# Performance work log

Hardware: AMD Instinct MI355X
Metric: run time of the kernel (lower is better)

The kernel has to match this reference:

```python
import jax, jax.numpy as jnp
import numpy as np

DIM_MODEL = 1024
DIM_K = 1024
DIM_V = 1024


def setup_inputs() -> dict:
    key = jax.random.key(0)
    ks = jax.random.split(key, 7)
    B, S = 4, 2048
    scale = 1.0 / np.sqrt(DIM_MODEL)
    return {
        "x": jax.random.normal(ks[0], (B, S, DIM_MODEL), dtype=jnp.float32),
        # weights stored [in, out] (transpose of torch Linear.weight)
        "Wq": jax.random.normal(ks[1], (DIM_MODEL, DIM_K), dtype=jnp.float32) * scale,
        "Wk": jax.random.normal(ks[2], (DIM_MODEL, DIM_K), dtype=jnp.float32) * scale,
        "Wv": jax.random.normal(ks[3], (DIM_MODEL, DIM_V), dtype=jnp.float32) * scale,
        "Wo": jax.random.normal(ks[4], (DIM_V, DIM_MODEL), dtype=jnp.float32) * (1.0 / np.sqrt(DIM_V)),
        "ln2_gamma": jnp.ones((DIM_MODEL,), dtype=jnp.float32),
        "ln2_beta": jnp.zeros((DIM_MODEL,), dtype=jnp.float32),
    }


def _layernorm(x, gamma, beta, eps=1e-5):
    mu = jnp.mean(x, axis=-1, keepdims=True)
    var = jnp.var(x, axis=-1, keepdims=True)
    return (x - mu) * jax.lax.rsqrt(var + eps) * gamma + beta


def reference(x, Wq, Wk, Wv, Wo, ln2_gamma, ln2_beta):
    # single-head attention, x: [B,S,D]
    q = jnp.einsum("bsd,dk->bsk", x, Wq)
    k = jnp.einsum("bsd,dk->bsk", x, Wk)
    v = jnp.einsum("bsd,dv->bsv", x, Wv)
    scores = jnp.einsum("bqk,bsk->bqs", q, k) / jnp.sqrt(jnp.asarray(DIM_K, x.dtype))
    attn = jax.nn.softmax(scores, axis=-1)  # [B,S,S]
    ctx = jnp.einsum("bqs,bsv->bqv", attn, v)
    hidden = jnp.einsum("bqv,vd->bqd", ctx, Wo)
    hidden = _layernorm(hidden, ln2_gamma, ln2_beta)
    return hidden
```

## Files before the change

### kernel.cpp

```cpp
#include <hip/hip_runtime.h>
#include <hip/hip_bf16.h>
#include <stdint.h>

typedef __bf16 bf16;
typedef __attribute__((ext_vector_type(8))) __bf16 bf16x8;
typedef __attribute__((ext_vector_type(4))) __bf16 bf16x4;
typedef __attribute__((ext_vector_type(4))) float f32x4;

#define AS1 __attribute__((address_space(1)))
#define AS3 __attribute__((address_space(3)))

__device__ __forceinline__ void gl_lds16(const void* g, void* l) {
  __builtin_amdgcn_global_load_lds((const AS1 uint32_t*)g, (AS3 uint32_t*)l, 16, 0, 0);
}

#define FENCE() asm volatile("" ::: "memory")
#define BAR()                        \
  do {                               \
    FENCE();                         \
    __builtin_amdgcn_s_barrier();    \
    FENCE();                         \
  } while (0)
#define VMW4() asm volatile("s_waitcnt vmcnt(4)" ::: "memory")

template <int MODE>
__global__ __launch_bounds__(512, 2) void gemm256(
    const bf16* __restrict__ Abase, const bf16* __restrict__ Bbase,
    bf16* __restrict__ Cbase, int K, int lda, int ldb, int ldc,
    long long sA, long long sB, long long sC, float alpha,
    float* __restrict__ lsum, bf16* __restrict__ C2, bf16* __restrict__ C3) {
  extern __shared__ char smem[];
  const int z = blockIdx.z;
  const bf16* A = Abase + (long long)z * sA;
  const bf16* B = Bbase + (long long)z * sB;
  bf16* C = Cbase + (long long)z * sC;
  const int m0 = blockIdx.y * 256, n0 = blockIdx.x * 256;
  const int t = threadIdx.x;
  const int lane = t & 63;
  const int wid = t >> 6, wrow = wid >> 2, wcol = wid & 3;
  const int quad = lane >> 4, r = lane & 15;

  const int rowq = t >> 3;
  const int chunk = (t & 7) ^ (rowq & 7);
  const bf16* pA0 = A + (long long)(m0 + rowq) * lda + chunk * 8;
  const bf16* pB0 = B + (long long)(n0 + rowq) * ldb + chunk * 8;

  const int aoff = (wrow * 64 + r) * 128;
  const int boff = 32768 + (wcol * 32 + r) * 128;
  const int cs0 = ((quad) ^ (r & 7)) * 16;
  const int cs1 = ((4 + quad) ^ (r & 7)) * 16;

#define STAGE_A(HALF, KT, SB)                                                  \
  do {                                                                         \
    gl_lds16(pA0 + (long long)((HALF) * 128) * lda + (KT),                     \
             (SB) + (HALF) * 16384 + t * 16);                                  \
    gl_lds16(pA0 + (long long)((HALF) * 128 + 64) * lda + (KT),                \
             (SB) + (HALF) * 16384 + 8192 + t * 16);                           \
  } while (0)
#define STAGE_B(HALF, KT, SB)                                                  \
  do {                                                                         \
    gl_lds16(pB0 + (long long)((HALF) * 128) * ldb + (KT),                     \
             (SB) + 32768 + (HALF) * 16384 + t * 16);                          \
    gl_lds16(pB0 + (long long)((HALF) * 128 + 64) * ldb + (KT),                \
             (SB) + 32768 + (HALF) * 16384 + 8192 + t * 16);                   \
  } while (0)
#define READ_A(MH)                                                             \
  _Pragma("unroll") for (int mr = 0; mr < 4; ++mr) {                           \
    af[mr][0] = *(const bf16x8*)(Sc + (MH) * 16384 + aoff + mr * 2048 + cs0);  \
    af[mr][1] = *(const bf16x8*)(Sc + (MH) * 16384 + aoff + mr * 2048 + cs1);  \
  }
#define READ_B(NH)                                                             \
  _Pragma("unroll") for (int nr = 0; nr < 2; ++nr) {                           \
    bfr[NH][nr][0] =                                                           \
        *(const bf16x8*)(Sc + (NH) * 16384 + boff + nr * 2048 + cs0);          \
    bfr[NH][nr][1] =                                                           \
        *(const bf16x8*)(Sc + (NH) * 16384 + boff + nr * 2048 + cs1);          \
  }
#define MMA(MH, NH)                                                            \
  _Pragma("unroll") for (int mr = 0; mr < 4; ++mr)                             \
      _Pragma("unroll") for (int nr = 0; nr < 2; ++nr) {                       \
    acc[MH][NH][mr][nr] = __builtin_amdgcn_mfma_f32_16x16x32_bf16(             \
        af[mr][0], bfr[NH][nr][0], acc[MH][NH][mr][nr], 0, 0, 0);              \
    acc[MH][NH][mr][nr] = __builtin_amdgcn_mfma_f32_16x16x32_bf16(             \
        af[mr][1], bfr[NH][nr][1], acc[MH][NH][mr][nr], 0, 0, 0);              \
  }

  f32x4 acc[2][2][4][2] = {};
  bf16x8 af[4][2];
  bf16x8 bfr[2][2][2];
  char* Sc = smem;
  char* Sn = smem + 65536;
  const int T = K >> 6;

  STAGE_A(0, 0, Sc);
  STAGE_B(0, 0, Sc);
  STAGE_A(1, 0, Sc);
  STAGE_B(1, 0, Sc);
  {
    const int kt1p = (T > 1) ? 64 : 0;
    STAGE_A(0, kt1p, Sn);
    STAGE_B(0, kt1p, Sn);
  }
  VMW4();
  BAR();

  for (int tt = 0; tt < T; ++tt) {
    const int kt1 = (tt + 1 < T ? tt + 1 : 0) << 6;
    const int kt2 = (tt + 2 < T ? tt + 2 : 0) << 6;
    READ_A(0);
    READ_B(0);
    STAGE_A(1, kt1, Sn);
    __builtin_amdgcn_s_setprio(1);
    MMA(0, 0);
    __builtin_amdgcn_s_setprio(0);
    BAR();
    READ_B(1);
    STAGE_B(1, kt1, Sn);
    __builtin_amdgcn_s_setprio(1);
    MMA(0, 1);
    __builtin_amdgcn_s_setprio(0);
    BAR();
    READ_A(1);
    STAGE_A(0, kt2, Sc);
    __builtin_amdgcn_s_setprio(1);
    MMA(1, 0);
    __builtin_amdgcn_s_setprio(0);
    BAR();
    STAGE_B(0, kt2, Sc);
    __builtin_amdgcn_s_setprio(1);
    MMA(1, 1);
    __builtin_amdgcn_s_setprio(0);
    VMW4();
    BAR();
    char* tp = Sc;
    Sc = Sn;
    Sn = tp;
  }

  if constexpr (MODE == 4) {
    bf16* dst;
    int c0;
    if (n0 < 1024) {
      dst = Cbase;
      c0 = n0;
    } else if (n0 < 2048) {
      dst = C2;
      c0 = n0 - 1024;
    } else {
      dst = C3;
      c0 = n0 - 2048;
    }
#pragma unroll
    for (int mh = 0; mh < 2; ++mh)
#pragma unroll
      for (int mr = 0; mr < 4; ++mr) {
        const int row0 = m0 + mh * 128 + wrow * 64 + mr * 16 + quad * 4;
#pragma unroll
        for (int nh = 0; nh < 2; ++nh)
#pragma unroll
          for (int nr = 0; nr < 2; ++nr) {
            const int col = c0 + nh * 128 + wcol * 32 + nr * 16 + r;
#pragma unroll
            for (int rg = 0; rg < 4; ++rg)
              dst[(long long)(row0 + rg) * 1024 + col] =
                  (bf16)acc[mh][nh][mr][nr][rg];
          }
      }
    return;
  }

#pragma unroll
  for (int mh = 0; mh < 2; ++mh)
#pragma unroll
    for (int mr = 0; mr < 4; ++mr) {
      const int row0 = m0 + mh * 128 + wrow * 64 + mr * 16 + quad * 4;
      float rsum[4] = {0.f, 0.f, 0.f, 0.f};
      float inv[4];
      if constexpr (MODE == 2) {
#pragma unroll
        for (int rg = 0; rg < 4; ++rg)
          inv[rg] = 1.f / lsum[(long long)z * 2048 + row0 + rg];
      }
#pragma unroll
      for (int nh = 0; nh < 2; ++nh)
#pragma unroll
        for (int nr = 0; nr < 2; ++nr) {
          const int col = n0 + nh * 128 + wcol * 32 + nr * 16 + r;
#pragma unroll
          for (int rg = 0; rg < 4; ++rg) {
            float v = acc[mh][nh][mr][nr][rg] * alpha;
            if constexpr (MODE == 1) {
              bf16 eb = (bf16)__expf(v);
              C[(long long)(row0 + rg) * ldc + col] = eb;
              rsum[rg] += (float)eb;
            } else if constexpr (MODE == 2) {
              C[(long long)(row0 + rg) * ldc + col] = (bf16)(v * inv[rg]);
            } else {
              C[(long long)(row0 + rg) * ldc + col] = (bf16)v;
            }
          }
        }
      if constexpr (MODE == 1) {
#pragma unroll
        for (int rg = 0; rg < 4; ++rg) {
#pragma unroll
          for (int off = 8; off >= 1; off >>= 1)
            rsum[rg] += __shfl_xor(rsum[rg], off);
          if (r == 0)
            atomicAdd(&lsum[(long long)z * 2048 + row0 + rg], rsum[rg]);
        }
      }
    }
#undef STAGE_A
#undef STAGE_B
#undef READ_A
#undef READ_B
#undef MMA
}

template <int MODE>
__global__ __launch_bounds__(256) void gemm128(
    const bf16* __restrict__ Abase, const bf16* __restrict__ Bbase,
    bf16* __restrict__ Cbase, int K, int lda, int ldb, int ldc,
    long long sA, long long sB, long long sC, float alpha,
    float* __restrict__ lsum, bf16* __restrict__ C2, bf16* __restrict__ C3) {
  extern __shared__ char smem[];
  const int z = blockIdx.z;
  const bf16* A = Abase + (long long)z * sA;
  const bf16* B = Bbase + (long long)z * sB;
  bf16* C = Cbase + (long long)z * sC;
  const int m0 = blockIdx.y * 128, n0 = blockIdx.x * 128;
  const int t = threadIdx.x;
  const int lane = t & 63, wave = t >> 6;
  const int wm = (wave >> 1) * 64, wn = (wave & 1) * 64;
  const int quad = lane >> 4, r = lane & 15;

  const int srow = t >> 3;
  const int schunk = (t & 7) ^ (srow & 7);
  const bf16* ga = A + (long long)(m0 + srow) * lda + schunk * 8;
  const bf16* gb = B + (long long)(n0 + srow) * ldb + schunk * 8;
  char* la = smem + t * 16;
  char* lb = smem + 16384 + t * 16;

  f32x4 acc[4][4] = {};

  for (int k0 = 0; k0 < K; k0 += 64) {
    __syncthreads();
#pragma unroll
    for (int rd = 0; rd < 4; rd++) {
      gl_lds16(ga + (long long)(32 * rd) * lda, la + rd * 4096);
      gl_lds16(gb + (long long)(32 * rd) * ldb, lb + rd * 4096);
    }
    ga += 64;
    gb += 64;
    __syncthreads();

#pragma unroll
    for (int kk = 0; kk < 2; kk++) {
      bf16x8 af[4], bfr[4];
      const int csa = ((kk * 4 + quad) ^ (r & 7)) * 16;
      const char* pa = smem + (wm + r) * 128 + csa;
      const char* pb = smem + 16384 + (wn + r) * 128 + csa;
#pragma unroll
      for (int i = 0; i < 4; i++) af[i] = *(const bf16x8*)(pa + i * 2048);
#pragma unroll
      for (int j = 0; j < 4; j++) bfr[j] = *(const bf16x8*)(pb + j * 2048);
#pragma unroll
      for (int i = 0; i < 4; i++)
#pragma unroll
        for (int j = 0; j < 4; j++)
          acc[i][j] = __builtin_amdgcn_mfma_f32_16x16x32_bf16(af[i], bfr[j],
                                                              acc[i][j], 0, 0, 0);
    }
  }

#pragma unroll
  for (int i = 0; i < 4; i++) {
    const int row0 = m0 + wm + i * 16 + quad * 4;
#pragma unroll
    for (int j = 0; j < 4; j++) {
      const int col = n0 + wn + j * 16 + r;
#pragma unroll
      for (int rg = 0; rg < 4; rg++) {
        float v = acc[i][j][rg] * alpha;
        C[(long long)(row0 + rg) * ldc + col] = (bf16)v;
      }
    }
  }
}

__global__ __launch_bounds__(256) void prep(
    const float* __restrict__ x, const float* __restrict__ Wq,
    const float* __restrict__ Wk, const float* __restrict__ Wv,
    const float* __restrict__ Wo, bf16* __restrict__ Xb,
    bf16* __restrict__ Wcat, bf16* __restrict__ Wot,
    float* __restrict__ lsum) {
  __shared__ float tile[32][33];
  const int bx = blockIdx.x;
  const int t = threadIdx.x;
  if (bx < 4096) {
    if (bx < 32) lsum[bx * 256 + t] = 0.f;
    long long i = (long long)bx * 256 + t;
    const float4* p = (const float4*)x;
    float4 a = p[i * 2], b = p[i * 2 + 1];
    bf16x8 o;
    o[0] = (bf16)a.x; o[1] = (bf16)a.y; o[2] = (bf16)a.z; o[3] = (bf16)a.w;
    o[4] = (bf16)b.x; o[5] = (bf16)b.y; o[6] = (bf16)b.z; o[7] = (bf16)b.w;
    ((bf16x8*)Xb)[i] = o;
  } else {
    int idx = bx - 4096;
    const int zw = idx >> 10;
    idx &= 1023;
    const int tiy = idx >> 5, tix = idx & 31;
    const float* W = (zw == 0) ? Wq : (zw == 1) ? Wk : (zw == 2) ? Wv : Wo;
    bf16* dst = (zw < 3) ? (Wcat + (long long)zw * 1024 * 1024) : Wot;
    const int bx0 = tix * 32, by0 = tiy * 32;
    const int ttx = t & 31, tty = t >> 5;
#pragma unroll
    for (int i = 0; i < 32; i += 8)
      tile[tty + i][ttx] = W[(long long)(by0 + tty + i) * 1024 + bx0 + ttx];
    __syncthreads();
#pragma unroll
    for (int i = 0; i < 32; i += 8)
      dst[(long long)(bx0 + tty + i) * 1024 + by0 + ttx] = (bf16)tile[ttx][tty + i];
  }
}

__global__ __launch_bounds__(256) void layernorm_rows(
    const bf16* __restrict__ H, const float* __restrict__ gamma,
    const float* __restrict__ beta, float* __restrict__ O) {
  const long long row = blockIdx.x;
  const bf16* h = H + row * 1024;
  float* o = O + row * 1024;
  const int t = threadIdx.x;
  const int lane = t & 63, wave = t >> 6;
  bf16x4 hv = ((const bf16x4*)h)[t];
  float v[4] = {(float)hv[0], (float)hv[1], (float)hv[2], (float)hv[3]};
  float s = v[0] + v[1] + v[2] + v[3];
  float ss = v[0] * v[0] + v[1] * v[1] + v[2] * v[2] + v[3] * v[3];
#pragma unroll
  for (int off = 32; off >= 1; off >>= 1) {
    s += __shfl_xor(s, off);
    ss += __shfl_xor(ss, off);
  }
  __shared__ float rs[4], rss[4];
  if (lane == 0) {
    rs[wave] = s;
    rss[wave] = ss;
  }
  __syncthreads();
  s = rs[0] + rs[1] + rs[2] + rs[3];
  ss = rss[0] + rss[1] + rss[2] + rss[3];
  const float mean = s * (1.f / 1024.f);
  const float var = ss * (1.f / 1024.f) - mean * mean;
  const float rstd = rsqrtf(var + 1e-5f);
  float4 g = ((const float4*)gamma)[t];
  float4 bb = ((const float4*)beta)[t];
  float4 rr;
  rr.x = (v[0] - mean) * rstd * g.x + bb.x;
  rr.y = (v[1] - mean) * rstd * g.y + bb.y;
  rr.z = (v[2] - mean) * rstd * g.z + bb.z;
  rr.w = (v[3] - mean) * rstd * g.w + bb.w;
  ((float4*)o)[t] = rr;
}

extern "C" void kernel_launch(void* const* d_in, const int* in_sizes, int n_in,
                              void* d_out, int out_size, void* d_ws,
                              size_t ws_size, hipStream_t stream) {
  const float* x = (const float*)d_in[0];
  const float* Wq = (const float*)d_in[1];
  const float* Wk = (const float*)d_in[2];
  const float* Wv = (const float*)d_in[3];
  const float* Wo = (const float*)d_in[4];
  const float* gamma = (const float*)d_in[5];
  const float* beta = (const float*)d_in[6];
  float* out = (float*)d_out;

  char* ws = (char*)d_ws;
  const size_t MB = 1024ull * 1024ull;
  bf16* Xb = (bf16*)(ws + 0);
  bf16* Wcat = (bf16*)(ws + 16 * MB);
  bf16* Wot = (bf16*)(ws + 22 * MB);
  bf16* Qd = (bf16*)(ws + 24 * MB);
  bf16* Kd = (bf16*)(ws + 40 * MB);
  bf16* Vd = (bf16*)(ws + 56 * MB);
  bf16* expS = (bf16*)(ws + 72 * MB);
  float* lsum = (float*)(ws + 104 * MB);
  bf16* VWo = (bf16*)(ws + 105 * MB);
  bf16* Hd = (bf16*)(ws + 121 * MB);

  static int inited = 0;
  if (!inited) {
    hipFuncSetAttribute(reinterpret_cast<const void*>(&gemm256<4>),
                        hipFuncAttributeMaxDynamicSharedMemorySize, 131072);
    hipFuncSetAttribute(reinterpret_cast<const void*>(&gemm256<1>),
                        hipFuncAttributeMaxDynamicSharedMemorySize, 131072);
    hipFuncSetAttribute(reinterpret_cast<const void*>(&gemm256<2>),
                        hipFuncAttributeMaxDynamicSharedMemorySize, 131072);
    inited = 1;
  }

  prep<<<8192, 256, 0, stream>>>(x, Wq, Wk, Wv, Wo, Xb, Wcat, Wot, lsum);

  gemm256<4><<<dim3(12, 32, 1), 512, 131072, stream>>>(
      Xb, Wcat, Qd, 1024, 1024, 1024, 1024, 0, 0, 0, 1.f, nullptr, Kd, Vd);

  gemm256<1><<<dim3(8, 8, 4), 512, 131072, stream>>>(
      Qd, Kd, expS, 1024, 1024, 1024, 2048, 2048 * 1024LL, 2048 * 1024LL,
      2048 * 2048LL, 0.03125f, lsum, nullptr, nullptr);

  gemm128<0><<<dim3(16, 8, 4), 256, 32768, stream>>>(
      Wot, Vd, VWo, 1024, 1024, 1024, 2048, 0, 2048 * 1024LL, 1024 * 2048LL,
      1.f, nullptr, nullptr, nullptr);

  gemm256<2><<<dim3(4, 8, 4), 512, 131072, stream>>>(
      expS, VWo, Hd, 2048, 2048, 2048, 1024, 2048 * 2048LL, 1024 * 2048LL,
      2048 * 1024LL, 1.f, lsum, nullptr, nullptr);

  layernorm_rows<<<8192, 256, 0, stream>>>(Hd, gamma, beta, out);
}
```

Measured before the change: 279.8 us.

## Fold Wv·Wo into a fused weight and project V·Wo inside the QKV GEMM

Precomputes the weight product Wv·Wo once, which is small, and writes it as the third block of the concatenated QKV weight. The projection GEMM then emits U = x·(Wv·Wo) directly in transposed layout. This removes the separate per-batch V·Wo GEMM, which was 2x the FLOPs. The QKV projection and the final P·U GEMM move from the 256-tile kernel to the 128-tile kernel with launch bounds set to 3 blocks, giving more blocks on this grid. Rounding Wv·Wo to bf16 adds a different rounding error, and the transposed bf16x4 stores are strided.

```diff
diff --git a/kernel.cpp b/kernel.cpp
--- a/kernel.cpp
+++ b/kernel.cpp
@@ -137,50 +137,12 @@
     Sn = tp;
   }
 
-  if constexpr (MODE == 4) {
-    bf16* dst;
-    int c0;
-    if (n0 < 1024) {
-      dst = Cbase;
-      c0 = n0;
-    } else if (n0 < 2048) {
-      dst = C2;
-      c0 = n0 - 1024;
-    } else {
-      dst = C3;
-      c0 = n0 - 2048;
-    }
-#pragma unroll
-    for (int mh = 0; mh < 2; ++mh)
-#pragma unroll
-      for (int mr = 0; mr < 4; ++mr) {
-        const int row0 = m0 + mh * 128 + wrow * 64 + mr * 16 + quad * 4;
-#pragma unroll
-        for (int nh = 0; nh < 2; ++nh)
-#pragma unroll
-          for (int nr = 0; nr < 2; ++nr) {
-            const int col = c0 + nh * 128 + wcol * 32 + nr * 16 + r;
-#pragma unroll
-            for (int rg = 0; rg < 4; ++rg)
-              dst[(long long)(row0 + rg) * 1024 + col] =
-                  (bf16)acc[mh][nh][mr][nr][rg];
-          }
-      }
-    return;
-  }
-
 #pragma unroll
   for (int mh = 0; mh < 2; ++mh)
 #pragma unroll
     for (int mr = 0; mr < 4; ++mr) {
       const int row0 = m0 + mh * 128 + wrow * 64 + mr * 16 + quad * 4;
       float rsum[4] = {0.f, 0.f, 0.f, 0.f};
-      float inv[4];
-      if constexpr (MODE == 2) {
-#pragma unroll
-        for (int rg = 0; rg < 4; ++rg)
-          inv[rg] = 1.f / lsum[(long long)z * 2048 + row0 + rg];
-      }
 #pragma unroll
       for (int nh = 0; nh < 2; ++nh)
 #pragma unroll
@@ -193,8 +155,6 @@
               bf16 eb = (bf16)__expf(v);
               C[(long long)(row0 + rg) * ldc + col] = eb;
               rsum[rg] += (float)eb;
-            } else if constexpr (MODE == 2) {
-              C[(long long)(row0 + rg) * ldc + col] = (bf16)(v * inv[rg]);
             } else {
               C[(long long)(row0 + rg) * ldc + col] = (bf16)v;
             }
@@ -219,7 +179,7 @@
 }
 
 template <int MODE>
-__global__ __launch_bounds__(256) void gemm128(
+__global__ __launch_bounds__(256, 3) void gemm128(
     const bf16* __restrict__ Abase, const bf16* __restrict__ Bbase,
     bf16* __restrict__ Cbase, int K, int lda, int ldb, int ldc,
     long long sA, long long sB, long long sC, float alpha,
@@ -274,16 +234,67 @@
     }
   }
 
+  if constexpr (MODE == 4) {
+    if (n0 >= 2048) {
+      bf16* Ut = C3;
+      const int d0 = n0 - 2048;
+#pragma unroll
+      for (int i = 0; i < 4; i++) {
+        const int s0 = m0 + wm + i * 16 + quad * 4;
+#pragma unroll
+        for (int j = 0; j < 4; j++) {
+          const int d = d0 + wn + j * 16 + r;
+          bf16x4 o;
+          o[0] = (bf16)acc[i][j][0];
+          o[1] = (bf16)acc[i][j][1];
+          o[2] = (bf16)acc[i][j][2];
+          o[3] = (bf16)acc[i][j][3];
+          *(bf16x4*)&Ut[(long long)d * 8192 + s0] = o;
+        }
+      }
+      return;
+    }
+    bf16* dst;
+    int c0;
+    if (n0 < 1024) {
+      dst = Cbase; c0 = n0;
+    } else {
+      dst = C2; c0 = n0 - 1024;
+    }
+#pragma unroll
+    for (int i = 0; i < 4; i++) {
+      const int row0 = m0 + wm + i * 16 + quad * 4;
+#pragma unroll
+      for (int j = 0; j < 4; j++) {
+        const int col = c0 + wn + j * 16 + r;
+#pragma unroll
+        for (int rg = 0; rg < 4; rg++)
+          dst[(long long)(row0 + rg) * 1024 + col] = (bf16)acc[i][j][rg];
+      }
+    }
+    return;
+  }
+
 #pragma unroll
   for (int i = 0; i < 4; i++) {
     const int row0 = m0 + wm + i * 16 + quad * 4;
+    float inv[4];
+    if constexpr (MODE == 2) {
+#pragma unroll
+      for (int rg = 0; rg < 4; rg++)
+        inv[rg] = 1.f / lsum[(long long)z * 2048 + row0 + rg];
+    }
 #pragma unroll
     for (int j = 0; j < 4; j++) {
       const int col = n0 + wn + j * 16 + r;
 #pragma unroll
       for (int rg = 0; rg < 4; rg++) {
         float v = acc[i][j][rg] * alpha;
-        C[(long long)(row0 + rg) * ldc + col] = (bf16)v;
+        if constexpr (MODE == 2) {
+          C[(long long)(row0 + rg) * ldc + col] = (bf16)(v * inv[rg]);
+        } else {
+          C[(long long)(row0 + rg) * ldc + col] = (bf16)v;
+        }
       }
     }
   }
@@ -294,7 +305,7 @@
     const float* __restrict__ Wk, const float* __restrict__ Wv,
     const float* __restrict__ Wo, bf16* __restrict__ Xb,
     bf16* __restrict__ Wcat, bf16* __restrict__ Wot,
-    float* __restrict__ lsum) {
+    bf16* __restrict__ Wvb, float* __restrict__ lsum) {
   __shared__ float tile[32][33];
   const int bx = blockIdx.x;
   const int t = threadIdx.x;
@@ -311,9 +322,17 @@
     int idx = bx - 4096;
     const int zw = idx >> 10;
     idx &= 1023;
+    if (zw == 2) {
+      const long long base = (long long)idx * 1024 + t * 4;
+      float4 v = *(const float4*)&Wv[base];
+      bf16x4 o;
+      o[0] = (bf16)v.x; o[1] = (bf16)v.y; o[2] = (bf16)v.z; o[3] = (bf16)v.w;
+      *(bf16x4*)&Wvb[base] = o;
+      return;
+    }
     const int tiy = idx >> 5, tix = idx & 31;
-    const float* W = (zw == 0) ? Wq : (zw == 1) ? Wk : (zw == 2) ? Wv : Wo;
-    bf16* dst = (zw < 3) ? (Wcat + (long long)zw * 1024 * 1024) : Wot;
+    const float* W = (zw == 0) ? Wq : (zw == 1) ? Wk : Wo;
+    bf16* dst = (zw == 0) ? Wcat : (zw == 1) ? (Wcat + 1024 * 1024) : Wot;
     const int bx0 = tix * 32, by0 = tiy * 32;
     const int ttx = t & 31, tty = t >> 5;
 #pragma unroll
@@ -383,38 +402,34 @@
   bf16* Wot = (bf16*)(ws + 22 * MB);
   bf16* Qd = (bf16*)(ws + 24 * MB);
   bf16* Kd = (bf16*)(ws + 40 * MB);
-  bf16* Vd = (bf16*)(ws + 56 * MB);
+  bf16* Ut = (bf16*)(ws + 56 * MB);
   bf16* expS = (bf16*)(ws + 72 * MB);
   float* lsum = (float*)(ws + 104 * MB);
-  bf16* VWo = (bf16*)(ws + 105 * MB);
+  bf16* Wvb = (bf16*)(ws + 105 * MB);
   bf16* Hd = (bf16*)(ws + 121 * MB);
 
   static int inited = 0;
   if (!inited) {
-    hipFuncSetAttribute(reinterpret_cast<const void*>(&gemm256<4>),
-                        hipFuncAttributeMaxDynamicSharedMemorySize, 131072);
     hipFuncSetAttribute(reinterpret_cast<const void*>(&gemm256<1>),
                         hipFuncAttributeMaxDynamicSharedMemorySize, 131072);
-    hipFuncSetAttribute(reinterpret_cast<const void*>(&gemm256<2>),
-                        hipFuncAttributeMaxDynamicSharedMemorySize, 131072);
     inited = 1;
   }
 
-  prep<<<8192, 256, 0, stream>>>(x, Wq, Wk, Wv, Wo, Xb, Wcat, Wot, lsum);
-
-  gemm256<4><<<dim3(12, 32, 1), 512, 131072, stream>>>(
-      Xb, Wcat, Qd, 1024, 1024, 1024, 1024, 0, 0, 0, 1.f, nullptr, Kd, Vd);
+  prep<<<8192, 256, 0, stream>>>(x, Wq, Wk, Wv, Wo, Xb, Wcat, Wot, Wvb, lsum);
+
+  gemm128<0><<<dim3(8, 8, 1), 256, 32768, stream>>>(
+      Wot, Wvb, Wcat + 2 * 1024 * 1024, 1024, 1024, 1024, 1024, 0, 0, 0, 1.f,
+      nullptr, nullptr, nullptr);
+
+  gemm128<4><<<dim3(24, 64, 1), 256, 32768, stream>>>(
+      Xb, Wcat, Qd, 1024, 1024, 1024, 1024, 0, 0, 0, 1.f, nullptr, Kd, Ut);
 
   gemm256<1><<<dim3(8, 8, 4), 512, 131072, stream>>>(
       Qd, Kd, expS, 1024, 1024, 1024, 2048, 2048 * 1024LL, 2048 * 1024LL,
       2048 * 2048LL, 0.03125f, lsum, nullptr, nullptr);
 
-  gemm128<0><<<dim3(16, 8, 4), 256, 32768, stream>>>(
-      Wot, Vd, VWo, 1024, 1024, 1024, 2048, 0, 2048 * 1024LL, 1024 * 2048LL,
-      1.f, nullptr, nullptr, nullptr);
-
-  gemm256<2><<<dim3(4, 8, 4), 512, 131072, stream>>>(
-      expS, VWo, Hd, 2048, 2048, 2048, 1024, 2048 * 2048LL, 1024 * 2048LL,
+  gemm128<2><<<dim3(8, 16, 4), 256, 32768, stream>>>(
+      expS, Ut, Hd, 2048, 2048, 8192, 1024, 2048 * 2048LL, 2048LL,
       2048 * 1024LL, 1.f, lsum, nullptr, nullptr);
 
   layernorm_rows<<<8192, 256, 0, stream>>>(Hd, gamma, beta, out);
```

Result: faster. 271.4 us (-3.0%).
